# Optimization experiments

Measured on AMD Instinct MI355X. Metric: run time of the kernel, lower is better.

The kernel has to match this reference:

```python
import jax, jax.numpy as jnp
import numpy as np

B, N, IN_DIM, OUT_DIM, K = 64, 256, 512, 512, 8
DK = OUT_DIM // K  # per-kernel feature dim


def setup_inputs() -> dict:
    key = jax.random.key(0)
    k1, k2, k3, k4 = jax.random.split(key, 4)
    node_feats = jax.random.normal(k1, (B, N, IN_DIM), dtype=jnp.float32)
    adj = jax.random.uniform(k2, (B, K, N, N), dtype=jnp.float32)
    weight = jax.random.normal(k3, (IN_DIM, OUT_DIM), dtype=jnp.float32) * (1.0 / np.sqrt(IN_DIM))
    bias = jax.random.normal(k4, (OUT_DIM,), dtype=jnp.float32) * 0.01
    return {"node_feats": node_feats, "adj": adj, "weight": weight, "bias": bias}


def reference(node_feats, adj, weight, bias):
    # kernel linear + ReLU: (b, n, out_dim)
    h = jax.nn.relu(jnp.einsum('bni,io->bno', node_feats, weight) + bias)
    # split into kernel slots: (b, n, k, dk)
    h = h.reshape(B, N, K, DK)
    # graph.aggregate: per-kernel dense message passing over adjacency
    # out[b,n,k,d] = sum_m adj[b,k,n,m] * h[b,m,k,d]
    agg = jnp.einsum('bknm,bmkd->bnkd', adj, h)
    return agg.reshape(B, N, OUT_DIM)
```

## Files before the change

kernel.cpp:

```cpp
#include <hip/hip_runtime.h>
#include <hip/hip_bf16.h>


typedef __attribute__((ext_vector_type(8))) short short8;
typedef __attribute__((ext_vector_type(4))) float floatx4;

__device__ __forceinline__ unsigned short f2bf(float f) {
    union { float f; unsigned u; } v; v.f = f;
    unsigned r = v.u + 0x7FFFu + ((v.u >> 16) & 1u);
    return (unsigned short)(r >> 16);
}

__device__ __forceinline__ unsigned pk2bf(float a, float b) {
    union { __hip_bfloat162 h; unsigned u; } cv;
    cv.h = __float22bfloat162_rn(make_float2(a, b));
    return cv.u;
}

__global__ __launch_bounds__(256) void wt_kernel(const float* __restrict__ W,
                                                 unsigned short* __restrict__ Wt) {
    __shared__ unsigned short t_lds[64 * 66];
    const int tile = blockIdx.x;
    const int k0 = (tile >> 3) * 64;
    const int o0 = (tile & 7) * 64;
    const int t = threadIdx.x;
    const int c = t & 63;
    const int rb = t >> 6;
#pragma unroll
    for (int i = 0; i < 16; ++i) {
        int r = i * 4 + rb;
        t_lds[c * 66 + r] = f2bf(W[(size_t)(k0 + r) * 512 + o0 + c]);
    }
    __syncthreads();
#pragma unroll
    for (int i = 0; i < 16; ++i) {
        int o_r = i * 4 + rb;
        Wt[(size_t)(o0 + o_r) * 512 + k0 + c] = t_lds[o_r * 66 + c];
    }
}

__global__ __launch_bounds__(512, 4) void fused_kernel(
    const float* __restrict__ X, const unsigned short* __restrict__ Wt,
    const float* __restrict__ bias, const float* __restrict__ adj,
    float* __restrict__ out) {
    __shared__ unsigned short ht[64 * 256];

    const int id = blockIdx.x;
    const int b = id & 63;
    const int ks = id >> 6;

    const int tid = threadIdx.x;
    const int lane = tid & 63, w = tid >> 6;
    const int lrow = lane & 15, quad = lane >> 4;
    const int m0 = w * 32;

    const float* Xb = X + (size_t)b * 256 * 512;
    const unsigned short* Wslice = Wt + (size_t)ks * 64 * 512;

    const float* xrow0 = Xb + (size_t)(m0 + lrow) * 512 + quad * 8;
    const float* xrow1 = xrow0 + 16 * 512;
    const unsigned short* wrow = Wslice + (size_t)lrow * 512 + quad * 8;

    float bv[4];
#pragma unroll
    for (int j = 0; j < 4; ++j) bv[j] = bias[ks * 64 + 16 * j + lrow];

    floatx4 acc1[2][4];
    const floatx4 fzero = {0.f, 0.f, 0.f, 0.f};
#pragma unroll
    for (int g = 0; g < 2; ++g)
#pragma unroll
        for (int j = 0; j < 4; ++j) acc1[g][j] = fzero;

    float4 xb_[2][2][2];
    short8 wb_[2][4];

#define LOAD_S1(buf, kb) do {                                           \
        const int k0_ = (kb) * 32;                                      \
        xb_[buf][0][0] = *(const float4*)(xrow0 + k0_);                 \
        xb_[buf][0][1] = *(const float4*)(xrow0 + k0_ + 4);             \
        xb_[buf][1][0] = *(const float4*)(xrow1 + k0_);                 \
        xb_[buf][1][1] = *(const float4*)(xrow1 + k0_ + 4);             \
        wb_[buf][0] = *(const short8*)(wrow + k0_);                     \
        wb_[buf][1] = *(const short8*)(wrow + 16 * 512 + k0_);          \
        wb_[buf][2] = *(const short8*)(wrow + 32 * 512 + k0_);          \
        wb_[buf][3] = *(const short8*)(wrow + 48 * 512 + k0_);          \
    } while (0)

    LOAD_S1(0, 0);
#pragma unroll
    for (int kb = 0; kb < 16; ++kb) {
        const int cur = kb & 1;
        if (kb < 15) LOAD_S1(cur ^ 1, kb + 1);
#pragma unroll
        for (int g = 0; g < 2; ++g) {
            union { short8 s; unsigned u[4]; } af;
            const float4 va = xb_[cur][g][0], vc = xb_[cur][g][1];
            af.u[0] = pk2bf(va.x, va.y);
            af.u[1] = pk2bf(va.z, va.w);
            af.u[2] = pk2bf(vc.x, vc.y);
            af.u[3] = pk2bf(vc.z, vc.w);
#pragma unroll
            for (int j = 0; j < 4; ++j)
                acc1[g][j] = __builtin_amdgcn_mfma_f32_16x16x32_bf16(
                    af.s, wb_[cur][j], acc1[g][j], 0, 0, 0);
        }
    }
#undef LOAD_S1

    const float* Abase = adj + ((size_t)(b * 8 + ks)) * 65536;
    const float* arow0 = Abase + (size_t)(m0 + lrow) * 256 + quad * 8;
    const float* arow1 = arow0 + 16 * 256;

    float4 ab_[2][2][2];
#define LOAD_S2(buf, mt) do {                                           \
        ab_[buf][0][0] = *(const float4*)(arow0 + (mt) * 32);           \
        ab_[buf][0][1] = *(const float4*)(arow0 + (mt) * 32 + 4);       \
        ab_[buf][1][0] = *(const float4*)(arow1 + (mt) * 32);           \
        ab_[buf][1][1] = *(const float4*)(arow1 + (mt) * 32 + 4);       \
    } while (0)

    LOAD_S2(0, 0);

#pragma unroll
    for (int g = 0; g < 2; ++g) {
#pragma unroll
        for (int j = 0; j < 4; ++j) {
            int d = 16 * j + lrow;
            floatx4 c = acc1[g][j];
            unsigned p01 = pk2bf(fmaxf(c.x + bv[j], 0.f), fmaxf(c.y + bv[j], 0.f));
            unsigned p23 = pk2bf(fmaxf(c.z + bv[j], 0.f), fmaxf(c.w + bv[j], 0.f));
            int jm = 4 * w + 2 * g + (quad >> 1);
            int phys = jm ^ (d & 7);
            unsigned* d32 = (unsigned*)(ht + d * 256 + phys * 8 + (quad & 1) * 4);
            d32[0] = p01; d32[1] = p23;
        }
    }
    __syncthreads();

    floatx4 acc2[2][4];
#pragma unroll
    for (int g = 0; g < 2; ++g)
#pragma unroll
        for (int j = 0; j < 4; ++j) acc2[g][j] = fzero;

#pragma unroll
    for (int mt = 0; mt < 8; ++mt) {
        const int cur = mt & 1;
        if (mt < 7) LOAD_S2(cur ^ 1, mt + 1);
        const int jm = 4 * mt + quad;
        short8 hfr[4];
#pragma unroll
        for (int dt = 0; dt < 4; ++dt) {
            int d = dt * 16 + lrow;
            hfr[dt] = *(const short8*)(ht + d * 256 + ((jm ^ (d & 7)) * 8));
        }
#pragma unroll
        for (int g = 0; g < 2; ++g) {
            union { short8 s; unsigned u[4]; } af;
            const float4 va = ab_[cur][g][0], vc = ab_[cur][g][1];
            af.u[0] = pk2bf(va.x, va.y);
            af.u[1] = pk2bf(va.z, va.w);
            af.u[2] = pk2bf(vc.x, vc.y);
            af.u[3] = pk2bf(vc.z, vc.w);
#pragma unroll
            for (int dt = 0; dt < 4; ++dt)
                acc2[g][dt] = __builtin_amdgcn_mfma_f32_16x16x32_bf16(
                    af.s, hfr[dt], acc2[g][dt], 0, 0, 0);
        }
    }
#undef LOAD_S2

#pragma unroll
    for (int g = 0; g < 2; ++g) {
        const int n_g = m0 + g * 16 + quad * 4;
        float* dst = out + ((size_t)b * 256 + n_g) * 512 + ks * 64 + lrow;
#pragma unroll
        for (int dt = 0; dt < 4; ++dt) {
            float* p = dst + dt * 16;
            p[0 * 512] = acc2[g][dt].x;
            p[1 * 512] = acc2[g][dt].y;
            p[2 * 512] = acc2[g][dt].z;
            p[3 * 512] = acc2[g][dt].w;
        }
    }
}

extern "C" void kernel_launch(void* const* d_in, const int* in_sizes, int n_in,
                              void* d_out, int out_size, void* d_ws, size_t ws_size,
                              hipStream_t stream) {
    const float* X    = (const float*)d_in[0];
    const float* adj  = (const float*)d_in[1];
    const float* W    = (const float*)d_in[2];
    const float* bias = (const float*)d_in[3];
    float* out = (float*)d_out;

    unsigned short* Wt = (unsigned short*)d_ws;

    wt_kernel<<<64, 256, 0, stream>>>(W, Wt);
    fused_kernel<<<512, 512, 0, stream>>>(X, Wt, bias, adj, out);
}
```

Baseline: 271.4 us.

## Stage X and adjacency tiles through LDS with coalesced row loads and swizzle

X and adjacency fragments are no longer loaded directly in MFMA fragment layout, which reads strided 32-byte chunks per lane. Each thread now loads a contiguous 64-byte half-row, converts it to bf16 once, and writes it into a double-buffered swizzled LDS tile. MFMA operands are then read from LDS. This is meant to improve global-load coalescing and remove redundant conversion work, at the cost of more LDS (32KB for ht plus 32KB of tiles), a barrier every k-step, and possibly lower occupancy.

After: 260.3 us. 1.04x faster.

```diff
diff --git a/kernel.cpp b/kernel.cpp
--- a/kernel.cpp
+++ b/kernel.cpp
@@ -43,7 +43,10 @@
     const float* __restrict__ X, const unsigned short* __restrict__ Wt,
     const float* __restrict__ bias, const float* __restrict__ adj,
     float* __restrict__ out) {
-    __shared__ unsigned short ht[64 * 256];
+    __shared__ struct {
+        unsigned short ht[64 * 256];
+        unsigned short tile[2][256 * 32];
+    } lds;
 
     const int id = blockIdx.x;
     const int b = id & 63;
@@ -52,14 +55,48 @@
     const int tid = threadIdx.x;
     const int lane = tid & 63, w = tid >> 6;
     const int lrow = lane & 15, quad = lane >> 4;
-    const int m0 = w * 32;
 
     const float* Xb = X + (size_t)b * 256 * 512;
     const unsigned short* Wslice = Wt + (size_t)ks * 64 * 512;
-
-    const float* xrow0 = Xb + (size_t)(m0 + lrow) * 512 + quad * 8;
-    const float* xrow1 = xrow0 + 16 * 512;
-    const unsigned short* wrow = Wslice + (size_t)lrow * 512 + quad * 8;
+    const float* Abase = adj + ((size_t)(b * 8 + ks)) * 65536;
+
+    const int srow = tid >> 1;
+    const int shalf = tid & 1;
+    const int sswz = (srow >> 1) & 3;
+    const int sd0 = srow * 32 + ((((shalf * 2)    ) ^ sswz) * 8);
+    const int sd1 = srow * 32 + ((((shalf * 2) + 1) ^ sswz) * 8);
+    const float* const xsrc = Xb + (size_t)srow * 512 + shalf * 16;
+    const float* const asrc = Abase + (size_t)srow * 256 + shalf * 16;
+
+#define LOADG(r, base, koff) do {                                       \
+        const float* s_ = (base) + (koff);                              \
+        r[0] = *(const float4*)(s_);                                    \
+        r[1] = *(const float4*)(s_ + 4);                                \
+        r[2] = *(const float4*)(s_ + 8);                                \
+        r[3] = *(const float4*)(s_ + 12);                               \
+    } while (0)
+
+#define WRITET(buf, r) do {                                             \
+        union { short8 s; unsigned u[4]; } t0_, t1_;                    \
+        t0_.u[0] = pk2bf(r[0].x, r[0].y); t0_.u[1] = pk2bf(r[0].z, r[0].w); \
+        t0_.u[2] = pk2bf(r[1].x, r[1].y); t0_.u[3] = pk2bf(r[1].z, r[1].w); \
+        t1_.u[0] = pk2bf(r[2].x, r[2].y); t1_.u[1] = pk2bf(r[2].z, r[2].w); \
+        t1_.u[2] = pk2bf(r[3].x, r[3].y); t1_.u[3] = pk2bf(r[3].z, r[3].w); \
+        *(short8*)(lds.tile[buf] + sd0) = t0_.s;                        \
+        *(short8*)(lds.tile[buf] + sd1) = t1_.s;                        \
+    } while (0)
+
+    int aoff[2];
+#pragma unroll
+    for (int g = 0; g < 2; ++g) {
+        int row = w * 32 + g * 16 + lrow;
+        aoff[g] = row * 32 + ((quad ^ ((row >> 1) & 3)) * 8);
+    }
+
+    const unsigned short* wptr[4];
+#pragma unroll
+    for (int ot = 0; ot < 4; ++ot)
+        wptr[ot] = Wslice + (size_t)(ot * 16 + lrow) * 512 + quad * 8;
 
     float bv[4];
 #pragma unroll
@@ -72,55 +109,38 @@
 #pragma unroll
         for (int j = 0; j < 4; ++j) acc1[g][j] = fzero;
 
-    float4 xb_[2][2][2];
-    short8 wb_[2][4];
-
-#define LOAD_S1(buf, kb) do {                                           \
-        const int k0_ = (kb) * 32;                                      \
-        xb_[buf][0][0] = *(const float4*)(xrow0 + k0_);                 \
-        xb_[buf][0][1] = *(const float4*)(xrow0 + k0_ + 4);             \
-        xb_[buf][1][0] = *(const float4*)(xrow1 + k0_);                 \
-        xb_[buf][1][1] = *(const float4*)(xrow1 + k0_ + 4);             \
-        wb_[buf][0] = *(const short8*)(wrow + k0_);                     \
-        wb_[buf][1] = *(const short8*)(wrow + 16 * 512 + k0_);          \
-        wb_[buf][2] = *(const short8*)(wrow + 32 * 512 + k0_);          \
-        wb_[buf][3] = *(const short8*)(wrow + 48 * 512 + k0_);          \
-    } while (0)
-
-    LOAD_S1(0, 0);
+    float4 xr[4];
+    short8 wfr[2][4];
+
+    LOADG(xr, xsrc, 0);
+    WRITET(0, xr);
+    LOADG(xr, xsrc, 32);
+#pragma unroll
+    for (int ot = 0; ot < 4; ++ot) wfr[0][ot] = *(const short8*)(wptr[ot]);
+    __syncthreads();
+
 #pragma unroll
     for (int kb = 0; kb < 16; ++kb) {
         const int cur = kb & 1;
-        if (kb < 15) LOAD_S1(cur ^ 1, kb + 1);
-#pragma unroll
-        for (int g = 0; g < 2; ++g) {
-            union { short8 s; unsigned u[4]; } af;
-            const float4 va = xb_[cur][g][0], vc = xb_[cur][g][1];
-            af.u[0] = pk2bf(va.x, va.y);
-            af.u[1] = pk2bf(va.z, va.w);
-            af.u[2] = pk2bf(vc.x, vc.y);
-            af.u[3] = pk2bf(vc.z, vc.w);
-#pragma unroll
-            for (int j = 0; j < 4; ++j)
-                acc1[g][j] = __builtin_amdgcn_mfma_f32_16x16x32_bf16(
-                    af.s, wb_[cur][j], acc1[g][j], 0, 0, 0);
-        }
-    }
-#undef LOAD_S1
-
-    const float* Abase = adj + ((size_t)(b * 8 + ks)) * 65536;
-    const float* arow0 = Abase + (size_t)(m0 + lrow) * 256 + quad * 8;
-    const float* arow1 = arow0 + 16 * 256;
-
-    float4 ab_[2][2][2];
-#define LOAD_S2(buf, mt) do {                                           \
-        ab_[buf][0][0] = *(const float4*)(arow0 + (mt) * 32);           \
-        ab_[buf][0][1] = *(const float4*)(arow0 + (mt) * 32 + 4);       \
-        ab_[buf][1][0] = *(const float4*)(arow1 + (mt) * 32);           \
-        ab_[buf][1][1] = *(const float4*)(arow1 + (mt) * 32 + 4);       \
-    } while (0)
-
-    LOAD_S2(0, 0);
+        if (kb < 15) {
+            WRITET(cur ^ 1, xr);
+#pragma unroll
+            for (int ot = 0; ot < 4; ++ot)
+                wfr[cur ^ 1][ot] = *(const short8*)(wptr[ot] + (kb + 1) * 32);
+        }
+        if (kb < 14) LOADG(xr, xsrc, (kb + 2) * 32);
+        short8 af0 = *(const short8*)(lds.tile[cur] + aoff[0]);
+        short8 af1 = *(const short8*)(lds.tile[cur] + aoff[1]);
+#pragma unroll
+        for (int ot = 0; ot < 4; ++ot) {
+            acc1[0][ot] = __builtin_amdgcn_mfma_f32_16x16x32_bf16(af0, wfr[cur][ot], acc1[0][ot], 0, 0, 0);
+            acc1[1][ot] = __builtin_amdgcn_mfma_f32_16x16x32_bf16(af1, wfr[cur][ot], acc1[1][ot], 0, 0, 0);
+        }
+        __syncthreads();
+    }
+
+    float4 ar[4];
+    LOADG(ar, asrc, 0);
 
 #pragma unroll
     for (int g = 0; g < 2; ++g) {
@@ -132,10 +152,12 @@
             unsigned p23 = pk2bf(fmaxf(c.z + bv[j], 0.f), fmaxf(c.w + bv[j], 0.f));
             int jm = 4 * w + 2 * g + (quad >> 1);
             int phys = jm ^ (d & 7);
-            unsigned* d32 = (unsigned*)(ht + d * 256 + phys * 8 + (quad & 1) * 4);
+            unsigned* d32 = (unsigned*)(lds.ht + d * 256 + phys * 8 + (quad & 1) * 4);
             d32[0] = p01; d32[1] = p23;
         }
     }
+    WRITET(0, ar);
+    LOADG(ar, asrc, 32);
     __syncthreads();
 
     floatx4 acc2[2][4];
@@ -147,33 +169,24 @@
 #pragma unroll
     for (int mt = 0; mt < 8; ++mt) {
         const int cur = mt & 1;
-        if (mt < 7) LOAD_S2(cur ^ 1, mt + 1);
-        const int jm = 4 * mt + quad;
-        short8 hfr[4];
+        if (mt < 7) WRITET(cur ^ 1, ar);
+        if (mt < 6) LOADG(ar, asrc, (mt + 2) * 32);
+        short8 af0 = *(const short8*)(lds.tile[cur] + aoff[0]);
+        short8 af1 = *(const short8*)(lds.tile[cur] + aoff[1]);
 #pragma unroll
         for (int dt = 0; dt < 4; ++dt) {
             int d = dt * 16 + lrow;
-            hfr[dt] = *(const short8*)(ht + d * 256 + ((jm ^ (d & 7)) * 8));
-        }
-#pragma unroll
-        for (int g = 0; g < 2; ++g) {
-            union { short8 s; unsigned u[4]; } af;
-            const float4 va = ab_[cur][g][0], vc = ab_[cur][g][1];
-            af.u[0] = pk2bf(va.x, va.y);
-            af.u[1] = pk2bf(va.z, va.w);
-            af.u[2] = pk2bf(vc.x, vc.y);
-            af.u[3] = pk2bf(vc.z, vc.w);
-#pragma unroll
-            for (int dt = 0; dt < 4; ++dt)
-                acc2[g][dt] = __builtin_amdgcn_mfma_f32_16x16x32_bf16(
-                    af.s, hfr[dt], acc2[g][dt], 0, 0, 0);
-        }
-    }
-#undef LOAD_S2
+            int jm = 4 * mt + quad;
+            short8 hf = *(const short8*)(lds.ht + d * 256 + ((jm ^ (d & 7)) * 8));
+            acc2[0][dt] = __builtin_amdgcn_mfma_f32_16x16x32_bf16(af0, hf, acc2[0][dt], 0, 0, 0);
+            acc2[1][dt] = __builtin_amdgcn_mfma_f32_16x16x32_bf16(af1, hf, acc2[1][dt], 0, 0, 0);
+        }
+        if (mt < 7) __syncthreads();
+    }
 
 #pragma unroll
     for (int g = 0; g < 2; ++g) {
-        const int n_g = m0 + g * 16 + quad * 4;
+        const int n_g = w * 32 + g * 16 + quad * 4;
         float* dst = out + ((size_t)b * 256 + n_g) * 512 + ks * 64 + lrow;
 #pragma unroll
         for (int dt = 0; dt < 4; ++dt) {
@@ -184,6 +197,8 @@
             p[3 * 512] = acc2[g][dt].w;
         }
     }
+#undef LOADG
+#undef WRITET
 }
 
 extern "C" void kernel_launch(void* const* d_in, const int* in_sizes, int n_in,
```
